# Optimization experiments

Measured on AMD Instinct MI355X. Metric: run time of the kernel, lower is better.

## Reference

```python
import jax, jax.numpy as jnp
import numpy as np

NUM_HEADS = 16


def setup_inputs() -> dict:
    key = jax.random.key(0)
    k1, k2, k3 = jax.random.split(key, 3)
    B, L, H = 2, 2048, 1024
    return {
        "key": jax.random.normal(k1, (B, L, H), dtype=jnp.float32),
        "W_ctx": jax.random.normal(k2, (H, H), dtype=jnp.float32) * (1.0 / np.sqrt(H)),
        "b_ctx": jax.random.normal(k3, (H,), dtype=jnp.float32) * 0.01,
    }


def reference(key, W_ctx, b_ctx):
    # Note: the torch module defines q/k/v Linear layers but never calls them
    # in forward(); it reshapes the raw input into heads directly.
    B, L, H = key.shape
    dh = H // NUM_HEADS
    # [B, L, H] -> [B, nh, L, dh]
    x = key.reshape(B, L, NUM_HEADS, dh).transpose(0, 2, 1, 3)
    # QK^T then scale by sqrt(head_dim) (key.shape[-1] after head split)
    scores = jnp.einsum("bhqd,bhkd->bhqk", x, x) * (1.0 / np.float32(np.sqrt(dh)))
    attn = jax.nn.softmax(scores, axis=-1)  # dropout p treated as eval/identity
    ctx = jnp.einsum("bhqk,bhkd->bhqd", attn, x)
    # [B, nh, L, dh] -> [B, L, H]
    ctx = ctx.transpose(0, 2, 1, 3).reshape(B, L, H)
    # context_transform: nn.Linear(H, H, bias=True)
    return ctx @ W_ctx.T + b_ctx
```

## Files before the change

### kernel.cpp

```cpp
#include <hip/hip_runtime.h>
#include <stdint.h>

#define NH     16
#define LSEQ   2048
#define DH     64
#define HDIM   1024
#define BATCH  2

typedef __attribute__((ext_vector_type(8))) short bf16x8;
typedef __attribute__((ext_vector_type(4))) short bf16x4;
typedef __attribute__((ext_vector_type(8))) unsigned short u16x8;
typedef __attribute__((ext_vector_type(4))) float f32x4;

static __device__ inline unsigned short f2bs(float f) {
    union { float f; uint32_t u; } v; v.f = f;
    uint32_t u = v.u;
    return (unsigned short)((u + 0x7FFFu + ((u >> 16) & 1u)) >> 16);
}
static __device__ inline float bf2f(unsigned short s) {
    return __uint_as_float(((uint32_t)s) << 16);
}

#define GLOAD_LDS(gp, lp) \
    __builtin_amdgcn_global_load_lds((const __attribute__((address_space(1))) void*)(gp), \
                                     (__attribute__((address_space(3))) void*)(lp), 16, 0, 0)

#define QK_SCALE 0.42466083f

__global__ __launch_bounds__(256) void cvt_kernel(const float* __restrict__ W,
                                                  unsigned short* __restrict__ wbt) {
    const int gid = blockIdx.x * 256 + threadIdx.x;
    const int n  = gid >> 7;
    const int kc = gid & 127;
    const float* src = W + (size_t)n * 1024 + kc * 8;
    float4 f0 = *(const float4*)(src);
    float4 f1 = *(const float4*)(src + 4);
    u16x8 v;
    v[0]=f2bs(f0.x); v[1]=f2bs(f0.y); v[2]=f2bs(f0.z); v[3]=f2bs(f0.w);
    v[4]=f2bs(f1.x); v[5]=f2bs(f1.y); v[6]=f2bs(f1.z); v[7]=f2bs(f1.w);
    const int nt = n >> 7, rn = n & 127;
    const int kt = kc >> 3, c = kc & 7;
    *(u16x8*)(wbt + (((size_t)nt * 16 + kt) * 128 + rn) * 64 + ((c ^ (rn & 7)) * 8)) = v;
}

__global__ __launch_bounds__(256) void xcvt_kernel(const float* __restrict__ x,
                                                   unsigned short* __restrict__ xb,
                                                   unsigned short* __restrict__ xt) {
    const int lt = blockIdx.x, bh = blockIdx.y;
    const int b = bh >> 4, h = bh & 15;
    const int t = threadIdx.x;
    const int r = t >> 2, cp = t & 3;

    __shared__ __align__(16) unsigned short Sm[64][72];

    const float* src = x + ((size_t)(b * LSEQ + lt * 64 + r)) * HDIM + h * DH + cp * 16;
    float4 f0 = *(const float4*)(src);
    float4 f1 = *(const float4*)(src + 4);
    float4 f2 = *(const float4*)(src + 8);
    float4 f3 = *(const float4*)(src + 12);
    u16x8 lo, hi;
    lo[0]=f2bs(f0.x); lo[1]=f2bs(f0.y); lo[2]=f2bs(f0.z); lo[3]=f2bs(f0.w);
    lo[4]=f2bs(f1.x); lo[5]=f2bs(f1.y); lo[6]=f2bs(f1.z); lo[7]=f2bs(f1.w);
    hi[0]=f2bs(f2.x); hi[1]=f2bs(f2.y); hi[2]=f2bs(f2.z); hi[3]=f2bs(f2.w);
    hi[4]=f2bs(f3.x); hi[5]=f2bs(f3.y); hi[6]=f2bs(f3.z); hi[7]=f2bs(f3.w);
    u16x8 slo, shi;
    slo[0]=f2bs(f0.x*QK_SCALE); slo[1]=f2bs(f0.y*QK_SCALE); slo[2]=f2bs(f0.z*QK_SCALE); slo[3]=f2bs(f0.w*QK_SCALE);
    slo[4]=f2bs(f1.x*QK_SCALE); slo[5]=f2bs(f1.y*QK_SCALE); slo[6]=f2bs(f1.z*QK_SCALE); slo[7]=f2bs(f1.w*QK_SCALE);
    shi[0]=f2bs(f2.x*QK_SCALE); shi[1]=f2bs(f2.y*QK_SCALE); shi[2]=f2bs(f2.z*QK_SCALE); shi[3]=f2bs(f2.w*QK_SCALE);
    shi[4]=f2bs(f3.x*QK_SCALE); shi[5]=f2bs(f3.y*QK_SCALE); shi[6]=f2bs(f3.z*QK_SCALE); shi[7]=f2bs(f3.w*QK_SCALE);

    {
        unsigned short* kt = xb + ((size_t)(bh * 32 + lt)) * 4096;
        const int s  = r >> 4, la = r & 15;
        const int ks = cp >> 1, q0 = (cp & 1) * 2;
        *(u16x8*)(kt + ((s * 2 + ks) * 64 + q0 * 16 + la) * 8)       = slo;
        *(u16x8*)(kt + ((s * 2 + ks) * 64 + (q0 + 1) * 16 + la) * 8) = shi;
    }
    *(u16x8*)&Sm[r][cp * 16]     = lo;
    *(u16x8*)&Sm[r][cp * 16 + 8] = hi;
    __syncthreads();

    {
        const int dt = t >> 6, lane = t & 63;
        const int la = lane & 15, quad = lane >> 4;
        u16x8 g0, g1;
        #pragma unroll
        for (int kvt = 0; kvt < 2; ++kvt)
            #pragma unroll
            for (int j = 0; j < 4; ++j)
                g0[kvt * 4 + j] = Sm[kvt * 16 + quad * 4 + j][dt * 16 + la];
        #pragma unroll
        for (int kvt = 0; kvt < 2; ++kvt)
            #pragma unroll
            for (int j = 0; j < 4; ++j)
                g1[kvt * 4 + j] = Sm[(kvt + 2) * 16 + quad * 4 + j][dt * 16 + la];
        unsigned short* vt = xt + ((size_t)(bh * 32 + lt)) * 4096;
        *(u16x8*)(vt + (dt * 64 + lane) * 16)     = g0;
        *(u16x8*)(vt + (dt * 64 + lane) * 16 + 8) = g1;
    }
}

__global__ __launch_bounds__(256) void attn_kernel(const unsigned short* __restrict__ xb,
                                                   const unsigned short* __restrict__ xt,
                                                   unsigned short* __restrict__ po,
                                                   float* __restrict__ pl,
                                                   int nt_tiles) {
    const int bh = blockIdx.x;
    const int qt = blockIdx.y;
    const int ksb = blockIdx.z;
    const int tid = threadIdx.x;
    const int w = tid >> 6, lane = tid & 63;
    const int la = lane & 15, quad = lane >> 4;

    __shared__ __align__(16) unsigned short KL[2][4096];
    __shared__ __align__(16) unsigned short VL[2][4096];

    const unsigned short* xbh = xb + (size_t)bh * 32 * 4096;
    const unsigned short* xth = xt + (size_t)bh * 32 * 4096;
    const int qbase = qt * 128 + w * 32;
    const int t0 = ksb * nt_tiles;

    bf16x8 qf[2][2];
    #pragma unroll
    for (int qnt = 0; qnt < 2; ++qnt) {
        const int q0 = qbase + qnt * 16;
        const unsigned short* qs = xbh + (q0 >> 6) * 4096 + (((q0 >> 4) & 3) * 2) * 512;
        qf[qnt][0] = *(const bf16x8*)(qs + lane * 8);
        qf[qnt][1] = *(const bf16x8*)(qs + 512 + lane * 8);
    }

    const f32x4 fzero = {0.f, 0.f, 0.f, 0.f};
    f32x4 acc[2][4];
    #pragma unroll
    for (int i = 0; i < 2; ++i)
        #pragma unroll
        for (int j = 0; j < 4; ++j) acc[i][j] = fzero;
    float lp[2] = {0.f, 0.f};

    #pragma unroll
    for (int j = 0; j < 2; ++j) {
        const int off = (j * 256 + tid) * 16;
        GLOAD_LDS((const char*)(xbh + t0 * 4096) + off, (char*)KL[0] + off);
        GLOAD_LDS((const char*)(xth + t0 * 4096) + off, (char*)VL[0] + off);
    }
    __syncthreads();

    for (int tt = 0; tt < nt_tiles; ++tt) {
        if (tt < nt_tiles - 1) {
            const char* ksrc = (const char*)(xbh + (t0 + tt + 1) * 4096);
            char* kdst = (char*)KL[(tt + 1) & 1];
            #pragma unroll
            for (int j = 0; j < 2; ++j) {
                const int off = (j * 256 + tid) * 16;
                GLOAD_LDS(ksrc + off, kdst + off);
            }
        }

        const unsigned short* kb = KL[tt & 1];
        f32x4 st[4][2];
        #pragma unroll
        for (int kvt = 0; kvt < 4; ++kvt) {
            bf16x8 kf0 = *(const bf16x8*)(kb + (kvt * 2 + 0) * 512 + lane * 8);
            bf16x8 kf1 = *(const bf16x8*)(kb + (kvt * 2 + 1) * 512 + lane * 8);
            #pragma unroll
            for (int qnt = 0; qnt < 2; ++qnt) {
                f32x4 s = fzero;
                s = __builtin_amdgcn_mfma_f32_16x16x32_bf16(kf0, qf[qnt][0], s, 0, 0, 0);
                s = __builtin_amdgcn_mfma_f32_16x16x32_bf16(kf1, qf[qnt][1], s, 0, 0, 0);
                st[kvt][qnt] = s;
            }
        }

        bf16x4 pf[2][4];
        #pragma unroll
        for (int qnt = 0; qnt < 2; ++qnt) {
            float ls = 0.f;
            #pragma unroll
            for (int kvt = 0; kvt < 4; ++kvt) {
                float p0 = __builtin_amdgcn_exp2f(st[kvt][qnt][0]);
                float p1 = __builtin_amdgcn_exp2f(st[kvt][qnt][1]);
                float p2 = __builtin_amdgcn_exp2f(st[kvt][qnt][2]);
                float p3 = __builtin_amdgcn_exp2f(st[kvt][qnt][3]);
                ls += (p0 + p1) + (p2 + p3);
                uint32_t u0 = __float_as_uint(p0) + 0x8000u;
                uint32_t u1 = __float_as_uint(p1) + 0x8000u;
                uint32_t u2 = __float_as_uint(p2) + 0x8000u;
                uint32_t u3 = __float_as_uint(p3) + 0x8000u;
                union { uint2 u; bf16x4 v; } cv;
                cv.u = make_uint2(__builtin_amdgcn_perm(u1, u0, 0x07060302),
                                  __builtin_amdgcn_perm(u3, u2, 0x07060302));
                pf[qnt][kvt] = cv.v;
            }
            lp[qnt] += ls;
        }

        __syncthreads();

        if (tt < nt_tiles - 1) {
            const char* vsrc = (const char*)(xth + (t0 + tt + 1) * 4096);
            char* vdst = (char*)VL[(tt + 1) & 1];
            #pragma unroll
            for (int j = 0; j < 2; ++j) {
                const int off = (j * 256 + tid) * 16;
                GLOAD_LDS(vsrc + off, vdst + off);
            }
        }

        const unsigned short* vb = VL[tt & 1];
        #pragma unroll
        for (int dt = 0; dt < 4; ++dt) {
            const unsigned short* vrow = vb + (dt * 64 + lane) * 16;
            #pragma unroll
            for (int kvt = 0; kvt < 4; ++kvt) {
                bf16x4 vf = *(const bf16x4*)(vrow + kvt * 4);
                #pragma unroll
                for (int qnt = 0; qnt < 2; ++qnt)
                    acc[qnt][dt] = __builtin_amdgcn_mfma_f32_16x16x16bf16_1k(
                        vf, pf[qnt][kvt], acc[qnt][dt], 0, 0, 0);
            }
        }
    }

    const size_t prow = (size_t)(ksb * 32 + bh) * 2048 + qbase;
    unsigned short* pob = po + prow * 64;
    #pragma unroll
    for (int qnt = 0; qnt < 2; ++qnt) {
        unsigned short* orow = pob + (size_t)(qnt * 16 + la) * 64 + quad * 4;
        #pragma unroll
        for (int dt = 0; dt < 4; ++dt) {
            f32x4 a = acc[qnt][dt];
            *(ushort4*)(orow + dt * 16) =
                make_ushort4(f2bs(a[0]), f2bs(a[1]), f2bs(a[2]), f2bs(a[3]));
        }
    }
    #pragma unroll
    for (int qnt = 0; qnt < 2; ++qnt) {
        float l = lp[qnt];
        l += __shfl_xor(l, 16);
        l += __shfl_xor(l, 32);
        if (quad == 0) pl[prow + qnt * 16 + la] = l;
    }
}

__global__ __launch_bounds__(256) void reduce_kernel(const unsigned short* __restrict__ po,
                                                     const float* __restrict__ pl,
                                                     unsigned short* __restrict__ ctxt,
                                                     int KS) {
    const int gid = blockIdx.x * 256 + threadIdx.x;
    const int rid = gid >> 4;
    const int d0  = (gid & 15) * 4;
    float l = 0.f;
    for (int s = 0; s < KS; ++s) l += pl[(size_t)s * 65536 + rid];
    const float invl = 1.0f / l;
    float o0 = 0.f, o1 = 0.f, o2 = 0.f, o3 = 0.f;
    for (int s = 0; s < KS; ++s) {
        ushort4 a = *(const ushort4*)(po + ((size_t)s * 65536 + rid) * 64 + d0);
        o0 += bf2f(a.x); o1 += bf2f(a.y); o2 += bf2f(a.z); o3 += bf2f(a.w);
    }
    const int bh = rid >> 11, q = rid & 2047;
    const int b = bh >> 4, h = bh & 15;
    const int m = b * 2048 + q;
    const int mt = m >> 7, r = m & 127;
    const int c = d0 >> 3, off = d0 & 7;
    unsigned short* dst = ctxt + (((size_t)mt * 16 + h) * 128 + r) * 64 + ((c ^ (r & 7)) * 8) + off;
    *(ushort4*)dst = make_ushort4(f2bs(o0 * invl), f2bs(o1 * invl),
                                  f2bs(o2 * invl), f2bs(o3 * invl));
}

__global__ __launch_bounds__(256) void proj_kernel(const unsigned short* __restrict__ ctxt,
                                                   const unsigned short* __restrict__ wbt,
                                                   const float* __restrict__ bias,
                                                   float* __restrict__ out) {
    const int ntb = blockIdx.x;
    const int mtb = blockIdx.y;
    const int tid = threadIdx.x;
    const int w = tid >> 6, lane = tid & 63;
    const int la = lane & 15, quad = lane >> 4;
    const int wm = (w >> 1) * 64, wn = (w & 1) * 64;

    __shared__ __align__(16) unsigned short As[2][8192];
    __shared__ __align__(16) unsigned short Bs[2][8192];

    const unsigned short* abase = ctxt + (size_t)mtb * 16 * 8192;
    const unsigned short* bbase = wbt  + (size_t)ntb * 16 * 8192;

    const int sw0 = ((quad)     ^ (la & 7)) * 8;
    const int sw1 = ((quad + 4) ^ (la & 7)) * 8;

    const f32x4 fzero = {0.f, 0.f, 0.f, 0.f};
    f32x4 acc[4][4];
    #pragma unroll
    for (int i = 0; i < 4; ++i)
        #pragma unroll
        for (int j = 0; j < 4; ++j) acc[i][j] = fzero;

    #pragma unroll
    for (int j = 0; j < 4; ++j) {
        const int fc = j * 256 + tid;
        GLOAD_LDS((const char*)abase + fc * 16, (char*)As[0] + fc * 16);
        GLOAD_LDS((const char*)bbase + fc * 16, (char*)Bs[0] + fc * 16);
    }
    __syncthreads();

    for (int kt = 0; kt < 16; ++kt) {
        if (kt < 15) {
            const char* asrc = (const char*)(abase + (kt + 1) * 8192);
            const char* bsrc = (const char*)(bbase + (kt + 1) * 8192);
            char* adst = (char*)As[(kt + 1) & 1];
            char* bdst = (char*)Bs[(kt + 1) & 1];
            #pragma unroll
            for (int j = 0; j < 4; ++j) {
                const int fc = j * 256 + tid;
                GLOAD_LDS(asrc + fc * 16, adst + fc * 16);
                GLOAD_LDS(bsrc + fc * 16, bdst + fc * 16);
            }
        }

        const unsigned short* Ab = As[kt & 1];
        const unsigned short* Bb = Bs[kt & 1];
        #pragma unroll
        for (int ks2 = 0; ks2 < 2; ++ks2) {
            const int sw = ks2 ? sw1 : sw0;
            bf16x8 af[4], bfr[4];
            #pragma unroll
            for (int mt = 0; mt < 4; ++mt) af[mt]  = *(const bf16x8*)&Ab[(wm + mt * 16 + la) * 64 + sw];
            #pragma unroll
            for (int nt = 0; nt < 4; ++nt) bfr[nt] = *(const bf16x8*)&Bb[(wn + nt * 16 + la) * 64 + sw];
            #pragma unroll
            for (int mt = 0; mt < 4; ++mt)
                #pragma unroll
                for (int nt = 0; nt < 4; ++nt)
                    acc[mt][nt] = __builtin_amdgcn_mfma_f32_16x16x32_bf16(af[mt], bfr[nt], acc[mt][nt], 0, 0, 0);
        }
        __syncthreads();
    }

    const int m0 = mtb * 128, n0 = ntb * 128;
    #pragma unroll
    for (int nt = 0; nt < 4; ++nt) {
        const int n = n0 + wn + nt * 16 + la;
        const float bv = bias[n];
        #pragma unroll
        for (int mt = 0; mt < 4; ++mt)
            #pragma unroll
            for (int r = 0; r < 4; ++r) {
                const int m = m0 + wm + mt * 16 + quad * 4 + r;
                out[(size_t)m * HDIM + n] = acc[mt][nt][r] + bv;
            }
    }
}

extern "C" void kernel_launch(void* const* d_in, const int* in_sizes, int n_in,
                              void* d_out, int out_size, void* d_ws, size_t ws_size,
                              hipStream_t stream) {
    const float* x    = (const float*)d_in[0];
    const float* W    = (const float*)d_in[1];
    const float* bias = (const float*)d_in[2];
    float* out = (float*)d_out;

    const int KS = (ws_size >= (60u << 20)) ? 4 : 2;

    unsigned short* ctxt = (unsigned short*)d_ws;
    unsigned short* xbp  = (unsigned short*)((char*)d_ws + ( 8u << 20));
    unsigned short* xtp  = (unsigned short*)((char*)d_ws + (16u << 20));
    unsigned short* wbt  = (unsigned short*)((char*)d_ws + (24u << 20));
    float*          pl   = (float*)         ((char*)d_ws + (26u << 20));
    unsigned short* po   = (unsigned short*)((char*)d_ws + (27u << 20));

    cvt_kernel<<<dim3(512), 256, 0, stream>>>(W, wbt);
    xcvt_kernel<<<dim3(32, 32), 256, 0, stream>>>(x, xbp, xtp);
    attn_kernel<<<dim3(32, 16, KS), 256, 0, stream>>>(xbp, xtp, po, pl, 32 / KS);
    reduce_kernel<<<dim3(4096), 256, 0, stream>>>(po, pl, ctxt, KS);
    proj_kernel<<<dim3(8, 32), 256, 0, stream>>>(ctxt, wbt, bias, out);
}
```

Measured before the change: 159.4 us.

## Drop split-KV reduction and fuse weight conversion into input prep kernel

Removes the KV-split in the attention kernel, so each block walks all 32 KV tiles and normalizes and writes the swizzled bf16 context directly, which eliminates the partial-output buffers and the separate reduce kernel. It also folds the weight fp32-to-bf16 conversion into the x conversion kernel, using half of each block's threads. The launch count drops from five to three and the partial-sum global traffic goes away. In exchange the attention grid shrinks from up to 2048 blocks to 512 with a longer serial loop per block, which may leave the GPU underfilled.

```diff
diff --git a/kernel.cpp b/kernel.cpp
--- a/kernel.cpp
+++ b/kernel.cpp
@@ -17,9 +17,6 @@
     uint32_t u = v.u;
     return (unsigned short)((u + 0x7FFFu + ((u >> 16) & 1u)) >> 16);
 }
-static __device__ inline float bf2f(unsigned short s) {
-    return __uint_as_float(((uint32_t)s) << 16);
-}
 
 #define GLOAD_LDS(gp, lp) \
     __builtin_amdgcn_global_load_lds((const __attribute__((address_space(1))) void*)(gp), \
@@ -27,28 +24,31 @@
 
 #define QK_SCALE 0.42466083f
 
-__global__ __launch_bounds__(256) void cvt_kernel(const float* __restrict__ W,
-                                                  unsigned short* __restrict__ wbt) {
-    const int gid = blockIdx.x * 256 + threadIdx.x;
-    const int n  = gid >> 7;
-    const int kc = gid & 127;
-    const float* src = W + (size_t)n * 1024 + kc * 8;
-    float4 f0 = *(const float4*)(src);
-    float4 f1 = *(const float4*)(src + 4);
-    u16x8 v;
-    v[0]=f2bs(f0.x); v[1]=f2bs(f0.y); v[2]=f2bs(f0.z); v[3]=f2bs(f0.w);
-    v[4]=f2bs(f1.x); v[5]=f2bs(f1.y); v[6]=f2bs(f1.z); v[7]=f2bs(f1.w);
-    const int nt = n >> 7, rn = n & 127;
-    const int kt = kc >> 3, c = kc & 7;
-    *(u16x8*)(wbt + (((size_t)nt * 16 + kt) * 128 + rn) * 64 + ((c ^ (rn & 7)) * 8)) = v;
-}
-
-__global__ __launch_bounds__(256) void xcvt_kernel(const float* __restrict__ x,
+__global__ __launch_bounds__(256) void prep_kernel(const float* __restrict__ x,
+                                                   const float* __restrict__ W,
                                                    unsigned short* __restrict__ xb,
-                                                   unsigned short* __restrict__ xt) {
+                                                   unsigned short* __restrict__ xt,
+                                                   unsigned short* __restrict__ wbt) {
     const int lt = blockIdx.x, bh = blockIdx.y;
+    const int bid = bh * 32 + lt;
+    const int t = threadIdx.x;
+
+    if (t < 128) {
+        const int gid = bid * 128 + t;
+        const int n  = gid >> 7;
+        const int kc = gid & 127;
+        const float* src = W + (size_t)n * 1024 + kc * 8;
+        float4 f0 = *(const float4*)(src);
+        float4 f1 = *(const float4*)(src + 4);
+        u16x8 v;
+        v[0]=f2bs(f0.x); v[1]=f2bs(f0.y); v[2]=f2bs(f0.z); v[3]=f2bs(f0.w);
+        v[4]=f2bs(f1.x); v[5]=f2bs(f1.y); v[6]=f2bs(f1.z); v[7]=f2bs(f1.w);
+        const int nt = n >> 7, rn = n & 127;
+        const int kt = kc >> 3, c = kc & 7;
+        *(u16x8*)(wbt + (((size_t)nt * 16 + kt) * 128 + rn) * 64 + ((c ^ (rn & 7)) * 8)) = v;
+    }
+
     const int b = bh >> 4, h = bh & 15;
-    const int t = threadIdx.x;
     const int r = t >> 2, cp = t & 3;
 
     __shared__ __align__(16) unsigned short Sm[64][72];
@@ -70,11 +70,11 @@
     shi[4]=f2bs(f3.x*QK_SCALE); shi[5]=f2bs(f3.y*QK_SCALE); shi[6]=f2bs(f3.z*QK_SCALE); shi[7]=f2bs(f3.w*QK_SCALE);
 
     {
-        unsigned short* kt = xb + ((size_t)(bh * 32 + lt)) * 4096;
-        const int s  = r >> 4, la = r & 15;
+        unsigned short* kt = xb + ((size_t)bid) * 4096;
+        const int s  = r >> 4, rla = r & 15;
         const int ks = cp >> 1, q0 = (cp & 1) * 2;
-        *(u16x8*)(kt + ((s * 2 + ks) * 64 + q0 * 16 + la) * 8)       = slo;
-        *(u16x8*)(kt + ((s * 2 + ks) * 64 + (q0 + 1) * 16 + la) * 8) = shi;
+        *(u16x8*)(kt + ((s * 2 + ks) * 64 + q0 * 16 + rla) * 8)       = slo;
+        *(u16x8*)(kt + ((s * 2 + ks) * 64 + (q0 + 1) * 16 + rla) * 8) = shi;
     }
     *(u16x8*)&Sm[r][cp * 16]     = lo;
     *(u16x8*)&Sm[r][cp * 16 + 8] = hi;
@@ -94,7 +94,7 @@
             #pragma unroll
             for (int j = 0; j < 4; ++j)
                 g1[kvt * 4 + j] = Sm[(kvt + 2) * 16 + quad * 4 + j][dt * 16 + la];
-        unsigned short* vt = xt + ((size_t)(bh * 32 + lt)) * 4096;
+        unsigned short* vt = xt + ((size_t)bid) * 4096;
         *(u16x8*)(vt + (dt * 64 + lane) * 16)     = g0;
         *(u16x8*)(vt + (dt * 64 + lane) * 16 + 8) = g1;
     }
@@ -102,12 +102,9 @@
 
 __global__ __launch_bounds__(256) void attn_kernel(const unsigned short* __restrict__ xb,
                                                    const unsigned short* __restrict__ xt,
-                                                   unsigned short* __restrict__ po,
-                                                   float* __restrict__ pl,
-                                                   int nt_tiles) {
+                                                   unsigned short* __restrict__ ctxt) {
     const int bh = blockIdx.x;
     const int qt = blockIdx.y;
-    const int ksb = blockIdx.z;
     const int tid = threadIdx.x;
     const int w = tid >> 6, lane = tid & 63;
     const int la = lane & 15, quad = lane >> 4;
@@ -118,7 +115,6 @@
     const unsigned short* xbh = xb + (size_t)bh * 32 * 4096;
     const unsigned short* xth = xt + (size_t)bh * 32 * 4096;
     const int qbase = qt * 128 + w * 32;
-    const int t0 = ksb * nt_tiles;
 
     bf16x8 qf[2][2];
     #pragma unroll
@@ -140,14 +136,14 @@
     #pragma unroll
     for (int j = 0; j < 2; ++j) {
         const int off = (j * 256 + tid) * 16;
-        GLOAD_LDS((const char*)(xbh + t0 * 4096) + off, (char*)KL[0] + off);
-        GLOAD_LDS((const char*)(xth + t0 * 4096) + off, (char*)VL[0] + off);
+        GLOAD_LDS((const char*)xbh + off, (char*)KL[0] + off);
+        GLOAD_LDS((const char*)xth + off, (char*)VL[0] + off);
     }
     __syncthreads();
 
-    for (int tt = 0; tt < nt_tiles; ++tt) {
-        if (tt < nt_tiles - 1) {
-            const char* ksrc = (const char*)(xbh + (t0 + tt + 1) * 4096);
+    for (int tt = 0; tt < 32; ++tt) {
+        if (tt < 31) {
+            const char* ksrc = (const char*)(xbh + (tt + 1) * 4096);
             char* kdst = (char*)KL[(tt + 1) & 1];
             #pragma unroll
             for (int j = 0; j < 2; ++j) {
@@ -196,8 +192,8 @@
 
         __syncthreads();
 
-        if (tt < nt_tiles - 1) {
-            const char* vsrc = (const char*)(xth + (t0 + tt + 1) * 4096);
+        if (tt < 31) {
+            const char* vsrc = (const char*)(xth + (tt + 1) * 4096);
             char* vdst = (char*)VL[(tt + 1) & 1];
             #pragma unroll
             for (int j = 0; j < 2; ++j) {
@@ -221,50 +217,26 @@
         }
     }
 
-    const size_t prow = (size_t)(ksb * 32 + bh) * 2048 + qbase;
-    unsigned short* pob = po + prow * 64;
-    #pragma unroll
-    for (int qnt = 0; qnt < 2; ++qnt) {
-        unsigned short* orow = pob + (size_t)(qnt * 16 + la) * 64 + quad * 4;
-        #pragma unroll
-        for (int dt = 0; dt < 4; ++dt) {
-            f32x4 a = acc[qnt][dt];
-            *(ushort4*)(orow + dt * 16) =
-                make_ushort4(f2bs(a[0]), f2bs(a[1]), f2bs(a[2]), f2bs(a[3]));
-        }
-    }
+    const int b = bh >> 4, h = bh & 15;
+    const int mt = b * 16 + qt;
+    unsigned short* tbase = ctxt + ((size_t)mt * 16 + h) * 128 * 64;
     #pragma unroll
     for (int qnt = 0; qnt < 2; ++qnt) {
         float l = lp[qnt];
         l += __shfl_xor(l, 16);
         l += __shfl_xor(l, 32);
-        if (quad == 0) pl[prow + qnt * 16 + la] = l;
-    }
-}
-
-__global__ __launch_bounds__(256) void reduce_kernel(const unsigned short* __restrict__ po,
-                                                     const float* __restrict__ pl,
-                                                     unsigned short* __restrict__ ctxt,
-                                                     int KS) {
-    const int gid = blockIdx.x * 256 + threadIdx.x;
-    const int rid = gid >> 4;
-    const int d0  = (gid & 15) * 4;
-    float l = 0.f;
-    for (int s = 0; s < KS; ++s) l += pl[(size_t)s * 65536 + rid];
-    const float invl = 1.0f / l;
-    float o0 = 0.f, o1 = 0.f, o2 = 0.f, o3 = 0.f;
-    for (int s = 0; s < KS; ++s) {
-        ushort4 a = *(const ushort4*)(po + ((size_t)s * 65536 + rid) * 64 + d0);
-        o0 += bf2f(a.x); o1 += bf2f(a.y); o2 += bf2f(a.z); o3 += bf2f(a.w);
-    }
-    const int bh = rid >> 11, q = rid & 2047;
-    const int b = bh >> 4, h = bh & 15;
-    const int m = b * 2048 + q;
-    const int mt = m >> 7, r = m & 127;
-    const int c = d0 >> 3, off = d0 & 7;
-    unsigned short* dst = ctxt + (((size_t)mt * 16 + h) * 128 + r) * 64 + ((c ^ (r & 7)) * 8) + off;
-    *(ushort4*)dst = make_ushort4(f2bs(o0 * invl), f2bs(o1 * invl),
-                                  f2bs(o2 * invl), f2bs(o3 * invl));
+        const float inv = 1.0f / l;
+        const int rr = w * 32 + qnt * 16 + la;
+        unsigned short* rowp = tbase + rr * 64 + (quad & 1) * 4;
+        #pragma unroll
+        for (int dt = 0; dt < 4; ++dt) {
+            f32x4 a = acc[qnt][dt];
+            const int c = dt * 2 + (quad >> 1);
+            *(ushort4*)(rowp + ((c ^ (rr & 7)) * 8)) =
+                make_ushort4(f2bs(a[0] * inv), f2bs(a[1] * inv),
+                             f2bs(a[2] * inv), f2bs(a[3] * inv));
+        }
+    }
 }
 
 __global__ __launch_bounds__(256) void proj_kernel(const unsigned short* __restrict__ ctxt,
@@ -358,18 +330,12 @@
     const float* bias = (const float*)d_in[2];
     float* out = (float*)d_out;
 
-    const int KS = (ws_size >= (60u << 20)) ? 4 : 2;
-
     unsigned short* ctxt = (unsigned short*)d_ws;
     unsigned short* xbp  = (unsigned short*)((char*)d_ws + ( 8u << 20));
     unsigned short* xtp  = (unsigned short*)((char*)d_ws + (16u << 20));
     unsigned short* wbt  = (unsigned short*)((char*)d_ws + (24u << 20));
-    float*          pl   = (float*)         ((char*)d_ws + (26u << 20));
-    unsigned short* po   = (unsigned short*)((char*)d_ws + (27u << 20));
-
-    cvt_kernel<<<dim3(512), 256, 0, stream>>>(W, wbt);
-    xcvt_kernel<<<dim3(32, 32), 256, 0, stream>>>(x, xbp, xtp);
-    attn_kernel<<<dim3(32, 16, KS), 256, 0, stream>>>(xbp, xtp, po, pl, 32 / KS);
-    reduce_kernel<<<dim3(4096), 256, 0, stream>>>(po, pl, ctxt, KS);
+
+    prep_kernel<<<dim3(32, 32), 256, 0, stream>>>(x, W, xbp, xtp, wbt);
+    attn_kernel<<<dim3(32, 16), 256, 0, stream>>>(xbp, xtp, ctxt);
     proj_kernel<<<dim3(8, 32), 256, 0, stream>>>(ctxt, wbt, bias, out);
 }
```

New measurement: 153.6 us. 3.7% less time.
